# Kernel tuning notes

Hardware: AMD Instinct MI355X
Metric: run time of the kernel (lower is better)

## Reference

```python
import jax, jax.numpy as jnp
import numpy as np

B, N, D, H = 2, 256, 512, 8
DK = D // H


def _lin(x, w, b):
    # torch nn.Linear: y = x @ W.T + b, W is [out, in]
    return jnp.matmul(x, w.T) + b


def setup_inputs() -> dict:
    key = jax.random.key(0)
    ks = jax.random.split(key, 12)
    std = 0.02
    inp = {
        "x": jax.random.normal(ks[0], (B, N, D), jnp.float32),
        "batched_graphs": jax.random.normal(ks[1], (B, N, N, D), jnp.float32) * std,
        "mask": jnp.zeros((B, N, N), dtype=bool),
    }
    names = ["wq", "wk", "wv", "wo", "wl", "wr", "wrk", "wrv"]
    for i, n in enumerate(names):
        inp[n] = jax.random.normal(ks[2 + i], (D, D), jnp.float32) * std
        inp["b" + n[1:]] = jnp.zeros((D,), jnp.float32)
    return inp


def reference(x, batched_graphs, mask,
              wq, bq, wk, bk, wv, bv, wo, bo,
              wl, bl, wr, br, wrk, brk, wrv, brv):
    # update_relations: per-edge key/value maps
    graphs_k = _lin(batched_graphs, wrk, brk).reshape(B, N, N, H, DK)
    graphs_v = _lin(batched_graphs, wrv, brv).reshape(B, N, N, H, DK)

    query = _lin(x, wq, bq).reshape(B, N, H, DK)
    key_ = _lin(x, wk, bk).reshape(B, N, H, DK)
    value = _lin(x, wv, bv).reshape(B, N, H, DK)

    scores_k = jnp.einsum("bxhd,byhd->bxyh", query, key_)
    scores_g = jnp.einsum("bxhd,bxyhd->bxyh", query, graphs_k)
    scores = (scores_k + scores_g) / np.sqrt(DK).astype(np.float32)
    scores = jnp.where(mask[..., None], jnp.float32(-1e9), scores)
    p_attn = jax.nn.softmax(scores, axis=2)  # over key nodes y

    x_v = jnp.einsum("bxyh,byhd->bxhd", p_attn, value)
    x_g = jnp.einsum("bxyh,bxyhd->bxhd", p_attn, graphs_v)
    out = (x_v + x_g).reshape(B, N, D)

    # relation update: outer sum of left/right projections
    x_left = _lin(out, wl, bl)[:, :, None, :]   # [B,N,1,D]
    x_right = _lin(out, wr, br)[:, None, :, :]  # [B,1,N,D]
    new_graphs = x_left + x_right               # [B,N,N,D]

    return _lin(out, wo, bo), new_graphs
```

## Files before the change

### kernel.cpp

```cpp
#include <hip/hip_runtime.h>

#define BB 2
#define NN 256
#define DD 512
#define HH 8

__device__ __forceinline__ float dot4(float4 a, float4 b) {
    return a.x*b.x + a.y*b.y + a.z*b.z + a.w*b.w;
}

__device__ __forceinline__ void gload_lds16(const void* g, void* l) {
    __builtin_amdgcn_global_load_lds(
        (const __attribute__((address_space(1))) unsigned int*)g,
        (__attribute__((address_space(3))) unsigned int*)l, 16, 0, 0);
}

__device__ __forceinline__ void stage_swz(const char* rowbase, float4* dst, int w, int lane) {
    #pragma unroll
    for (int j = 0; j < 4; ++j) {
        const int f0 = w * 256 + j * 64;
        const int y = f0 >> 7;
        const int c = (f0 & 127) + lane;
        gload_lds16(rowbase + (size_t)y * 2048 + ((size_t)(c ^ y) << 4), &dst[f0]);
    }
}

__global__ __launch_bounds__(256) void kProj(
    const float* __restrict__ in_,
    const float* __restrict__ w0, const float* __restrict__ b0,
    const float* __restrict__ w1, const float* __restrict__ b1,
    const float* __restrict__ w2, const float* __restrict__ b2,
    float* __restrict__ o0, float* __restrict__ o1, float* __restrict__ o2)
{
    __shared__ float4 xs[2][32 * 17];
    __shared__ float4 ws[2][32 * 17];

    const int t = threadIdx.x;
    const int blk = blockIdx.x;
    const int proj = blk >> 8;
    const int rem = blk & 255;
    const int row0 = (rem >> 4) * 32;
    const int col0 = (rem & 15) * 32;

    const float* W; const float* Bp; float* O;
    if (proj == 0)      { W = w0; Bp = b0; O = o0; }
    else if (proj == 1) { W = w1; Bp = b1; O = o1; }
    else                { W = w2; Bp = b2; O = o2; }

    const int sr0 = t >> 4,          se0 = t & 15;
    const int sr1 = (t + 256) >> 4,  se1 = t & 15;
    const float4* X4 = (const float4*)in_;
    const float4* W4 = (const float4*)W;

    float4 rx0 = X4[(size_t)(row0 + sr0) * 128 + se0];
    float4 rx1 = X4[(size_t)(row0 + sr1) * 128 + se1];
    float4 rw0 = W4[(size_t)(col0 + sr0) * 128 + se0];
    float4 rw1 = W4[(size_t)(col0 + sr1) * 128 + se1];
    xs[0][sr0 * 17 + se0] = rx0;
    xs[0][sr1 * 17 + se1] = rx1;
    ws[0][sr0 * 17 + se0] = rw0;
    ws[0][sr1 * 17 + se1] = rw1;

    const int ty = t >> 4, tx = t & 15;
    const int ra = 2 * ty, ca = 2 * tx;
    float a00 = 0, a01 = 0, a10 = 0, a11 = 0;

    for (int q = 0; q < 8; ++q) {
        __syncthreads();
        const int cur = q & 1;
        if (q < 7) {
            const int koff = (q + 1) * 16;
            rx0 = X4[(size_t)(row0 + sr0) * 128 + koff + se0];
            rx1 = X4[(size_t)(row0 + sr1) * 128 + koff + se1];
            rw0 = W4[(size_t)(col0 + sr0) * 128 + koff + se0];
            rw1 = W4[(size_t)(col0 + sr1) * 128 + koff + se1];
        }
        const float4* xb = xs[cur];
        const float4* wb = ws[cur];
        #pragma unroll
        for (int e4 = 0; e4 < 16; ++e4) {
            const float4 x0 = xb[ra * 17 + e4];
            const float4 x1 = xb[(ra + 1) * 17 + e4];
            const float4 v0 = wb[ca * 17 + e4];
            const float4 v1 = wb[(ca + 1) * 17 + e4];
            a00 += dot4(x0, v0); a01 += dot4(x0, v1);
            a10 += dot4(x1, v0); a11 += dot4(x1, v1);
        }
        if (q < 7) {
            const int nxt = cur ^ 1;
            xs[nxt][sr0 * 17 + se0] = rx0;
            xs[nxt][sr1 * 17 + se1] = rx1;
            ws[nxt][sr0 * 17 + se0] = rw0;
            ws[nxt][sr1 * 17 + se1] = rw1;
        }
    }

    const int orow = row0 + ra, ocol = col0 + ca;
    const float bx = Bp[ocol], by = Bp[ocol + 1];
    float2 s0; s0.x = a00 + bx; s0.y = a01 + by;
    float2 s1; s1.x = a10 + bx; s1.y = a11 + by;
    *(float2*)(O + (size_t)orow * DD + ocol) = s0;
    *(float2*)(O + (size_t)(orow + 1) * DD + ocol) = s1;
}

__global__ __launch_bounds__(256) void kQkp(
    const float* __restrict__ q, const float* __restrict__ wrk,
    float* __restrict__ qkp)
{
    __shared__ float qs[8 * 64];
    const int t = threadIdx.x;
    const int blk = blockIdx.x;
    const int rowg = blk >> 5;
    const int h = (blk >> 2) & 7;
    const int eq = blk & 3;
    const int row0 = rowg * 8;
    {
        const int r = t >> 5, d2 = (t & 31) * 2;
        const float2 tmp = *(const float2*)(q + (size_t)(row0 + r) * DD + h * 64 + d2);
        qs[r * 64 + d2] = tmp.x; qs[r * 64 + d2 + 1] = tmp.y;
    }
    __syncthreads();
    const int e = eq * 128 + (t & 127);
    const int rp = (t >> 7) * 4;
    const float* wcol = wrk + (size_t)(h * 64) * DD + e;
    float a0 = 0, a1 = 0, a2 = 0, a3 = 0;
    #pragma unroll 8
    for (int d = 0; d < 64; ++d) {
        const float wv = wcol[(size_t)d * DD];
        a0 += qs[(rp + 0) * 64 + d] * wv;
        a1 += qs[(rp + 1) * 64 + d] * wv;
        a2 += qs[(rp + 2) * 64 + d] * wv;
        a3 += qs[(rp + 3) * 64 + d] * wv;
    }
    qkp[((size_t)(row0 + rp + 0) * HH + h) * DD + e] = a0;
    qkp[((size_t)(row0 + rp + 1) * HH + h) * DD + e] = a1;
    qkp[((size_t)(row0 + rp + 2) * HH + h) * DD + e] = a2;
    qkp[((size_t)(row0 + rp + 3) * HH + h) * DD + e] = a3;
}

__global__ __launch_bounds__(256) void kSk(
    const float* __restrict__ q, const float* __restrict__ k,
    const unsigned char* __restrict__ mask, float* __restrict__ sk)
{
    __shared__ float qs[8 * 65];
    __shared__ float ks[64 * 65];
    const int t = threadIdx.x;
    const int blk = blockIdx.x;
    const int b  = blk >> 10;
    const int h  = (blk >> 7) & 7;
    const int xt = (blk >> 2) & 31;
    const int yt = blk & 3;
    const int x0 = xt * 8, y0 = yt * 64;
    {
        const int r = t >> 5, d2 = (t & 31) * 2;
        const float2 tmp = *(const float2*)(q + (size_t)(b * NN + x0 + r) * DD + h * 64 + d2);
        qs[r * 65 + d2] = tmp.x; qs[r * 65 + d2 + 1] = tmp.y;
    }
    #pragma unroll
    for (int j = 0; j < 8; ++j) {
        const int f = t + 256 * j;
        const int r = f >> 5, d2 = (f & 31) * 2;
        const float2 tmp = *(const float2*)(k + (size_t)(b * NN + y0 + r) * DD + h * 64 + d2);
        ks[r * 65 + d2] = tmp.x; ks[r * 65 + d2 + 1] = tmp.y;
    }
    __syncthreads();
    const int xi = t >> 5, yg = t & 31;
    float a0 = 0, a1 = 0;
    #pragma unroll 8
    for (int d = 0; d < 64; ++d) {
        const float qv = qs[xi * 65 + d];
        a0 += qv * ks[(yg * 2 + 0) * 65 + d];
        a1 += qv * ks[(yg * 2 + 1) * 65 + d];
    }
    a0 *= 0.125f; a1 *= 0.125f;
    const unsigned char* mrow = mask + (size_t)(b * NN + x0 + xi) * NN;
    const int gy = y0 + yg * 2;
    if (mrow[gy + 0]) a0 = -1e9f;
    if (mrow[gy + 1]) a1 = -1e9f;
    float2 st; st.x = a0; st.y = a1;
    *(float2*)(sk + ((size_t)(b * NN + x0 + xi) * HH + h) * NN + gy) = st;
}

__global__ __launch_bounds__(256) void kC(
    const float* __restrict__ G, const float* __restrict__ sk,
    const float* __restrict__ qkp, const float* __restrict__ v,
    float* __restrict__ pg, float* __restrict__ pxv,
    float* __restrict__ pm, float* __restrict__ pl)
{
    __shared__ float4 gbuf[2][1024];
    __shared__ float4 qk4[1024];
    __shared__ float s_l[64];

    const int t = threadIdx.x;
    const int lane = t & 63;
    const int w = t >> 6;
    const int blk = blockIdx.x;
    const int part = blk & 3;
    const int bid = blk >> 2;
    const int b = bid >> 8;
    const int ybase = part * 64;

    const char* Grow = (const char*)(G + (size_t)bid * NN * DD);
    stage_swz((const char*)(qkp + (size_t)bid * HH * DD), qk4, w, lane);
    stage_swz(Grow + (size_t)ybase * 2048, &gbuf[0][0], w, lane);
    __syncthreads();

    const int s_  = t & 15;
    const int h0i = ((t >> 4) & 3) * 2;
    const int y0i = w * 2;
    const int ec4 = t & 127;
    const int hb  = (t >> 7) * 4;
    const int hv  = t >> 5;
    const int d2  = (t & 31) * 2;

    float4 gacc0 = {0,0,0,0}, gacc1 = {0,0,0,0}, gacc2 = {0,0,0,0}, gacc3 = {0,0,0,0};
    float m0 = -3e38f, m1 = -3e38f, m2 = -3e38f, m3 = -3e38f;
    float l0 = 0, l1 = 0, l2 = 0, l3 = 0;
    float vx = 0, vy = 0, mvold = -3e38f;

    const float* vrow = v + (size_t)(b * NN + ybase) * DD + hv * 64 + d2;
    const float* skrow = sk + (size_t)bid * HH * NN;

    int cb = 0;
    for (int tt = 0; tt < 8; ++tt) {
        if (tt < 7)
            stage_swz(Grow + (size_t)(ybase + (tt + 1) * 8) * 2048, &gbuf[cb ^ 1][0], w, lane);

        {
            float a00 = 0, a01 = 0, a10 = 0, a11 = 0;
            const float4* gb = &gbuf[cb][0];
            #pragma unroll
            for (int i = 0; i < 8; ++i) {
                const int e4 = i * 16 + s_;
                const float4 g0 = gb[y0i * 128 + (e4 ^ y0i)];
                const float4 g1 = gb[(y0i + 1) * 128 + (e4 ^ (y0i + 1))];
                const float4 p0 = qk4[h0i * 128 + (e4 ^ h0i)];
                const float4 p1 = qk4[(h0i + 1) * 128 + (e4 ^ (h0i + 1))];
                a00 += dot4(g0, p0); a01 += dot4(g0, p1);
                a10 += dot4(g1, p0); a11 += dot4(g1, p1);
            }
            #pragma unroll
            for (int mm = 1; mm < 16; mm <<= 1) {
                a00 += __shfl_xor(a00, mm); a01 += __shfl_xor(a01, mm);
                a10 += __shfl_xor(a10, mm); a11 += __shfl_xor(a11, mm);
            }
            if (s_ < 4) {
                const int yy = s_ & 1, hh = s_ >> 1;
                const float val = yy ? (hh ? a11 : a10) : (hh ? a01 : a00);
                const int gy = ybase + tt * 8 + y0i + yy;
                const int h = h0i + hh;
                s_l[(y0i + yy) * 8 + h] = val * 0.125f + skrow[(size_t)h * NN + gy];
            }
        }
        __syncthreads();

        {
            {   const float tmx0 = fmaxf(fmaxf(fmaxf(s_l[0*8+hb+0], s_l[1*8+hb+0]), fmaxf(s_l[2*8+hb+0], s_l[3*8+hb+0])),
                                         fmaxf(fmaxf(s_l[4*8+hb+0], s_l[5*8+hb+0]), fmaxf(s_l[6*8+hb+0], s_l[7*8+hb+0])));
                const float mn = fmaxf(m0, tmx0); const float rs = __expf(m0 - mn);
                m0 = mn; l0 *= rs; gacc0.x *= rs; gacc0.y *= rs; gacc0.z *= rs; gacc0.w *= rs; }
            {   const float tmx1 = fmaxf(fmaxf(fmaxf(s_l[0*8+hb+1], s_l[1*8+hb+1]), fmaxf(s_l[2*8+hb+1], s_l[3*8+hb+1])),
                                         fmaxf(fmaxf(s_l[4*8+hb+1], s_l[5*8+hb+1]), fmaxf(s_l[6*8+hb+1], s_l[7*8+hb+1])));
                const float mn = fmaxf(m1, tmx1); const float rs = __expf(m1 - mn);
                m1 = mn; l1 *= rs; gacc1.x *= rs; gacc1.y *= rs; gacc1.z *= rs; gacc1.w *= rs; }
            {   const float tmx2 = fmaxf(fmaxf(fmaxf(s_l[0*8+hb+2], s_l[1*8+hb+2]), fmaxf(s_l[2*8+hb+2], s_l[3*8+hb+2])),
                                         fmaxf(fmaxf(s_l[4*8+hb+2], s_l[5*8+hb+2]), fmaxf(s_l[6*8+hb+2], s_l[7*8+hb+2])));
                const float mn = fmaxf(m2, tmx2); const float rs = __expf(m2 - mn);
                m2 = mn; l2 *= rs; gacc2.x *= rs; gacc2.y *= rs; gacc2.z *= rs; gacc2.w *= rs; }
            {   const float tmx3 = fmaxf(fmaxf(fmaxf(s_l[0*8+hb+3], s_l[1*8+hb+3]), fmaxf(s_l[2*8+hb+3], s_l[3*8+hb+3])),
                                         fmaxf(fmaxf(s_l[4*8+hb+3], s_l[5*8+hb+3]), fmaxf(s_l[6*8+hb+3], s_l[7*8+hb+3])));
                const float mn = fmaxf(m3, tmx3); const float rs = __expf(m3 - mn);
                m3 = mn; l3 *= rs; gacc3.x *= rs; gacc3.y *= rs; gacc3.z *= rs; gacc3.w *= rs; }

            const int ri = hv & 3;
            const float mv = (ri & 2) ? ((ri & 1) ? m3 : m2) : ((ri & 1) ? m1 : m0);
            const float rv = __expf(mvold - mv);
            vx *= rv; vy *= rv; mvold = mv;

            const float4* gb = &gbuf[cb][0];
            const float* vt = vrow + (size_t)tt * 8 * DD;
            #pragma unroll
            for (int y = 0; y < 8; ++y) {
                const float4 gv = gb[y * 128 + (ec4 ^ y)];
                const float2 vv = *(const float2*)(vt + (size_t)y * DD);
                const float p0 = __expf(s_l[y*8 + hb + 0] - m0); l0 += p0;
                gacc0.x += p0*gv.x; gacc0.y += p0*gv.y; gacc0.z += p0*gv.z; gacc0.w += p0*gv.w;
                const float p1 = __expf(s_l[y*8 + hb + 1] - m1); l1 += p1;
                gacc1.x += p1*gv.x; gacc1.y += p1*gv.y; gacc1.z += p1*gv.z; gacc1.w += p1*gv.w;
                const float p2 = __expf(s_l[y*8 + hb + 2] - m2); l2 += p2;
                gacc2.x += p2*gv.x; gacc2.y += p2*gv.y; gacc2.z += p2*gv.z; gacc2.w += p2*gv.w;
                const float p3 = __expf(s_l[y*8 + hb + 3] - m3); l3 += p3;
                gacc3.x += p3*gv.x; gacc3.y += p3*gv.y; gacc3.z += p3*gv.z; gacc3.w += p3*gv.w;
                const float pv = __expf(s_l[y*8 + hv] - mv);
                vx += pv * vv.x; vy += pv * vv.y;
            }
        }
        __syncthreads();
        cb ^= 1;
    }

    float4* pgb = (float4*)pg + (size_t)blk * 1024;
    pgb[(hb + 0) * 128 + ec4] = gacc0;
    pgb[(hb + 1) * 128 + ec4] = gacc1;
    pgb[(hb + 2) * 128 + ec4] = gacc2;
    pgb[(hb + 3) * 128 + ec4] = gacc3;
    float2 xvst; xvst.x = vx; xvst.y = vy;
    *(float2*)(pxv + (size_t)blk * DD + hv * 64 + d2) = xvst;
    if ((t & 127) == 0) {
        const int base = blk * 8 + hb;
        pm[base + 0] = m0; pm[base + 1] = m1; pm[base + 2] = m2; pm[base + 3] = m3;
        pl[base + 0] = l0; pl[base + 1] = l1; pl[base + 2] = l2; pl[base + 3] = l3;
    }
}

__global__ __launch_bounds__(256) void kM(
    const float* __restrict__ pg, const float* __restrict__ pxv,
    const float* __restrict__ pm, const float* __restrict__ pl,
    const float* __restrict__ wrv, const float* __restrict__ brv,
    float* __restrict__ om)
{
    __shared__ float4 gc[512];
    __shared__ float xvs[256];
    __shared__ float wexp[16], Ls[4];
    const int t = threadIdx.x;
    const int blk = blockIdx.x;
    const int bid = blk >> 1;
    const int half = blk & 1;
    const int h0 = half * 4;
    __shared__ float mlds[16], llds[16];
    if (t < 16) {
        const int i = t >> 2, hh = t & 3;
        mlds[t] = pm[bid * 32 + i * 8 + h0 + hh];
        llds[t] = pl[bid * 32 + i * 8 + h0 + hh];
    }
    __syncthreads();
    if (t < 4) {
        float M = mlds[t];
        #pragma unroll
        for (int i = 1; i < 4; ++i) M = fmaxf(M, mlds[i * 4 + t]);
        float L = 0;
        #pragma unroll
        for (int i = 0; i < 4; ++i) {
            const float wv = __expf(mlds[i * 4 + t] - M);
            wexp[i * 4 + t] = wv;
            L += wv * llds[i * 4 + t];
        }
        Ls[t] = L;
    }
    __syncthreads();
    const int c4 = t & 127;
    #pragma unroll
    for (int r = 0; r < 2; ++r) {
        const int hh = (t >> 7) * 2 + r;
        float4 acc = {0, 0, 0, 0};
        #pragma unroll
        for (int i = 0; i < 4; ++i) {
            const float wv = wexp[i * 4 + hh];
            const float4 g = ((const float4*)pg)[((size_t)bid * 4 + i) * 1024 + (size_t)(h0 + hh) * 128 + c4];
            acc.x += wv * g.x; acc.y += wv * g.y; acc.z += wv * g.z; acc.w += wv * g.w;
        }
        gc[hh * 128 + c4] = acc;
    }
    {
        const int hh = t >> 6;
        float s = 0;
        #pragma unroll
        for (int i = 0; i < 4; ++i)
            s += wexp[i * 4 + hh] * pxv[((size_t)bid * 4 + i) * DD + half * 256 + t];
        xvs[t] = s;
    }
    __syncthreads();
    const int o = half * 256 + t;
    const int hl = t >> 6;
    const float4* wr4 = (const float4*)(wrv + (size_t)o * DD);
    float acc = 0;
    #pragma unroll 4
    for (int e4 = 0; e4 < 128; ++e4) acc += dot4(wr4[e4], gc[hl * 128 + e4]);
    om[(size_t)bid * DD + o] = (xvs[t] + acc) / Ls[hl] + brv[o];
}

__global__ __launch_bounds__(256) void kE(
    const float* __restrict__ xl, const float* __restrict__ xr,
    float* __restrict__ ng)
{
    const int t = threadIdx.x;
    const int blk = blockIdx.x;
    const int bid = blk >> 2;
    const int yc = blk & 3;
    const int b = bid >> 8;
    const int o4 = t & 127;
    const int yh = t >> 7;
    const float4 left = ((const float4*)xl)[(size_t)bid * 128 + o4];
    const float4* xr4 = (const float4*)xr + (size_t)b * NN * 128;
    float4* out4 = (float4*)ng + (size_t)bid * NN * 128;
    for (int y = yc * 64 + yh; y < yc * 64 + 64; y += 2) {
        const float4 rr = xr4[y * 128 + o4];
        float4 s;
        s.x = left.x + rr.x; s.y = left.y + rr.y;
        s.z = left.z + rr.z; s.w = left.w + rr.w;
        out4[y * 128 + o4] = s;
    }
}

extern "C" void kernel_launch(void* const* d_in, const int* in_sizes, int n_in,
                              void* d_out, int out_size, void* d_ws, size_t ws_size,
                              hipStream_t stream)
{
    (void)in_sizes; (void)n_in; (void)out_size; (void)ws_size;
    const float* x    = (const float*)d_in[0];
    const float* G    = (const float*)d_in[1];
    const unsigned char* mask = (const unsigned char*)d_in[2];
    const float* wq  = (const float*)d_in[3];  const float* bq  = (const float*)d_in[4];
    const float* wk  = (const float*)d_in[5];  const float* bk  = (const float*)d_in[6];
    const float* wv  = (const float*)d_in[7];  const float* bv  = (const float*)d_in[8];
    const float* wo  = (const float*)d_in[9];  const float* bo  = (const float*)d_in[10];
    const float* wl  = (const float*)d_in[11]; const float* bl  = (const float*)d_in[12];
    const float* wr  = (const float*)d_in[13]; const float* br  = (const float*)d_in[14];
    const float* wrk = (const float*)d_in[15];
    const float* wrv = (const float*)d_in[17]; const float* brv = (const float*)d_in[18];

    float* out  = (float*)d_out;
    float* fout = out;
    float* ng   = out + (size_t)BB * NN * DD;

    const size_t ng_f  = (size_t)BB * NN * NN * DD;
    const size_t row_f = (size_t)BB * NN * DD;
    const size_t total = row_f * 52 + 32768;
    float* base = ng + ng_f - total;
    float* q    = base;
    float* k    = q   + row_f;
    float* vv_  = k   + row_f;
    float* qkp  = vv_ + row_f;
    float* skp  = qkp + row_f * 8;
    float* pg   = skp + row_f * 4;
    float* pxv  = pg  + row_f * 32;
    float* pm   = pxv + row_f * 4;
    float* pl   = pm  + 16384;
    float* om   = pl  + 16384;
    float* xl = (float*)d_ws;
    float* xr = xl + row_f;

    kProj<<<768, 256, 0, stream>>>(x, wq, bq, wk, bk, wv, bv, q, k, vv_);
    kQkp <<<2048, 256, 0, stream>>>(q, wrk, qkp);
    kSk  <<<2048, 256, 0, stream>>>(q, k, mask, skp);
    kC   <<<2048, 256, 0, stream>>>(G, skp, qkp, vv_, pg, pxv, pm, pl);
    kM   <<<1024, 256, 0, stream>>>(pg, pxv, pm, pl, wrv, brv, om);
    kProj<<<768, 256, 0, stream>>>(om, wo, bo, wl, bl, wr, br, fout, xl, xr);
    kE   <<<2048, 256, 0, stream>>>(xl, xr, ng);
}
```

Before: 301.6 us.

## Keep query-graph vectors in registers, reuse softmax exps, nontemporal graph stores

In the attention kernel, each thread now loads its query/relation-key slices from global memory into registers, replacing the shared-memory staging buffer and its extra sync. The V rows for each tile are loaded into registers ahead of the score phase. The value-path probability reuses the exponent already computed for its head instead of a separate exp and rescale. Tile scores are read from LDS as float4. The outer-sum kernel writes new_graphs with nontemporal stores so the large output streams past the cache. The trade-off is higher register pressure, which could lower occupancy.

```diff
diff --git a/kernel.cpp b/kernel.cpp
--- a/kernel.cpp
+++ b/kernel.cpp
@@ -5,8 +5,15 @@
 #define DD 512
 #define HH 8
 
+typedef float f4raw __attribute__((ext_vector_type(4)));
+
 __device__ __forceinline__ float dot4(float4 a, float4 b) {
     return a.x*b.x + a.y*b.y + a.z*b.z + a.w*b.w;
+}
+
+__device__ __forceinline__ float4 f4fma(float s, float4 a, float4 acc) {
+    acc.x += s * a.x; acc.y += s * a.y; acc.z += s * a.z; acc.w += s * a.w;
+    return acc;
 }
 
 __device__ __forceinline__ void gload_lds16(const void* g, void* l) {
@@ -188,7 +195,6 @@
     float* __restrict__ pm, float* __restrict__ pl)
 {
     __shared__ float4 gbuf[2][1024];
-    __shared__ float4 qk4[1024];
     __shared__ float s_l[64];
 
     const int t = threadIdx.x;
@@ -201,9 +207,7 @@
     const int ybase = part * 64;
 
     const char* Grow = (const char*)(G + (size_t)bid * NN * DD);
-    stage_swz((const char*)(qkp + (size_t)bid * HH * DD), qk4, w, lane);
     stage_swz(Grow + (size_t)ybase * 2048, &gbuf[0][0], w, lane);
-    __syncthreads();
 
     const int s_  = t & 15;
     const int h0i = ((t >> 4) & 3) * 2;
@@ -212,19 +216,36 @@
     const int hb  = (t >> 7) * 4;
     const int hv  = t >> 5;
     const int d2  = (t & 31) * 2;
+    const int ri  = hv & 3;
+
+    const float* qkpb = qkp + (size_t)bid * HH * DD;
+    float4 qv0[8], qv1[8];
+    #pragma unroll
+    for (int i = 0; i < 8; ++i) {
+        const int e4 = i * 16 + s_;
+        qv0[i] = *(const float4*)(qkpb + (size_t)h0i * DD + e4 * 4);
+        qv1[i] = *(const float4*)(qkpb + (size_t)(h0i + 1) * DD + e4 * 4);
+    }
 
     float4 gacc0 = {0,0,0,0}, gacc1 = {0,0,0,0}, gacc2 = {0,0,0,0}, gacc3 = {0,0,0,0};
     float m0 = -3e38f, m1 = -3e38f, m2 = -3e38f, m3 = -3e38f;
     float l0 = 0, l1 = 0, l2 = 0, l3 = 0;
-    float vx = 0, vy = 0, mvold = -3e38f;
+    float vx = 0, vy = 0;
 
     const float* vrow = v + (size_t)(b * NN + ybase) * DD + hv * 64 + d2;
     const float* skrow = sk + (size_t)bid * HH * NN;
+
+    __syncthreads();
 
     int cb = 0;
     for (int tt = 0; tt < 8; ++tt) {
         if (tt < 7)
             stage_swz(Grow + (size_t)(ybase + (tt + 1) * 8) * 2048, &gbuf[cb ^ 1][0], w, lane);
+
+        float2 vvs[8];
+        #pragma unroll
+        for (int y = 0; y < 8; ++y)
+            vvs[y] = *(const float2*)(vrow + ((size_t)tt * 8 + y) * DD);
 
         {
             float a00 = 0, a01 = 0, a10 = 0, a11 = 0;
@@ -234,10 +255,8 @@
                 const int e4 = i * 16 + s_;
                 const float4 g0 = gb[y0i * 128 + (e4 ^ y0i)];
                 const float4 g1 = gb[(y0i + 1) * 128 + (e4 ^ (y0i + 1))];
-                const float4 p0 = qk4[h0i * 128 + (e4 ^ h0i)];
-                const float4 p1 = qk4[(h0i + 1) * 128 + (e4 ^ (h0i + 1))];
-                a00 += dot4(g0, p0); a01 += dot4(g0, p1);
-                a10 += dot4(g1, p0); a11 += dot4(g1, p1);
+                a00 += dot4(g0, qv0[i]); a01 += dot4(g0, qv1[i]);
+                a10 += dot4(g1, qv0[i]); a11 += dot4(g1, qv1[i]);
             }
             #pragma unroll
             for (int mm = 1; mm < 16; mm <<= 1) {
@@ -254,45 +273,41 @@
         }
         __syncthreads();
 
+        float4 sv[8];
+        #pragma unroll
+        for (int y = 0; y < 8; ++y) sv[y] = *(const float4*)&s_l[y * 8 + hb];
+
+        float4 mx = sv[0];
+        #pragma unroll
+        for (int y = 1; y < 8; ++y) {
+            mx.x = fmaxf(mx.x, sv[y].x); mx.y = fmaxf(mx.y, sv[y].y);
+            mx.z = fmaxf(mx.z, sv[y].z); mx.w = fmaxf(mx.w, sv[y].w);
+        }
+        const float n0 = fmaxf(m0, mx.x), rs0 = __expf(m0 - n0);
+        const float n1 = fmaxf(m1, mx.y), rs1 = __expf(m1 - n1);
+        const float n2 = fmaxf(m2, mx.z), rs2 = __expf(m2 - n2);
+        const float n3 = fmaxf(m3, mx.w), rs3 = __expf(m3 - n3);
+        m0 = n0; m1 = n1; m2 = n2; m3 = n3;
+        l0 *= rs0; l1 *= rs1; l2 *= rs2; l3 *= rs3;
+        gacc0.x *= rs0; gacc0.y *= rs0; gacc0.z *= rs0; gacc0.w *= rs0;
+        gacc1.x *= rs1; gacc1.y *= rs1; gacc1.z *= rs1; gacc1.w *= rs1;
+        gacc2.x *= rs2; gacc2.y *= rs2; gacc2.z *= rs2; gacc2.w *= rs2;
+        gacc3.x *= rs3; gacc3.y *= rs3; gacc3.z *= rs3; gacc3.w *= rs3;
+        const float rsv = (ri == 0) ? rs0 : (ri == 1) ? rs1 : (ri == 2) ? rs2 : rs3;
+        vx *= rsv; vy *= rsv;
+
         {
-            {   const float tmx0 = fmaxf(fmaxf(fmaxf(s_l[0*8+hb+0], s_l[1*8+hb+0]), fmaxf(s_l[2*8+hb+0], s_l[3*8+hb+0])),
-                                         fmaxf(fmaxf(s_l[4*8+hb+0], s_l[5*8+hb+0]), fmaxf(s_l[6*8+hb+0], s_l[7*8+hb+0])));
-                const float mn = fmaxf(m0, tmx0); const float rs = __expf(m0 - mn);
-                m0 = mn; l0 *= rs; gacc0.x *= rs; gacc0.y *= rs; gacc0.z *= rs; gacc0.w *= rs; }
-            {   const float tmx1 = fmaxf(fmaxf(fmaxf(s_l[0*8+hb+1], s_l[1*8+hb+1]), fmaxf(s_l[2*8+hb+1], s_l[3*8+hb+1])),
-                                         fmaxf(fmaxf(s_l[4*8+hb+1], s_l[5*8+hb+1]), fmaxf(s_l[6*8+hb+1], s_l[7*8+hb+1])));
-                const float mn = fmaxf(m1, tmx1); const float rs = __expf(m1 - mn);
-                m1 = mn; l1 *= rs; gacc1.x *= rs; gacc1.y *= rs; gacc1.z *= rs; gacc1.w *= rs; }
-            {   const float tmx2 = fmaxf(fmaxf(fmaxf(s_l[0*8+hb+2], s_l[1*8+hb+2]), fmaxf(s_l[2*8+hb+2], s_l[3*8+hb+2])),
-                                         fmaxf(fmaxf(s_l[4*8+hb+2], s_l[5*8+hb+2]), fmaxf(s_l[6*8+hb+2], s_l[7*8+hb+2])));
-                const float mn = fmaxf(m2, tmx2); const float rs = __expf(m2 - mn);
-                m2 = mn; l2 *= rs; gacc2.x *= rs; gacc2.y *= rs; gacc2.z *= rs; gacc2.w *= rs; }
-            {   const float tmx3 = fmaxf(fmaxf(fmaxf(s_l[0*8+hb+3], s_l[1*8+hb+3]), fmaxf(s_l[2*8+hb+3], s_l[3*8+hb+3])),
-                                         fmaxf(fmaxf(s_l[4*8+hb+3], s_l[5*8+hb+3]), fmaxf(s_l[6*8+hb+3], s_l[7*8+hb+3])));
-                const float mn = fmaxf(m3, tmx3); const float rs = __expf(m3 - mn);
-                m3 = mn; l3 *= rs; gacc3.x *= rs; gacc3.y *= rs; gacc3.z *= rs; gacc3.w *= rs; }
-
-            const int ri = hv & 3;
-            const float mv = (ri & 2) ? ((ri & 1) ? m3 : m2) : ((ri & 1) ? m1 : m0);
-            const float rv = __expf(mvold - mv);
-            vx *= rv; vy *= rv; mvold = mv;
-
             const float4* gb = &gbuf[cb][0];
-            const float* vt = vrow + (size_t)tt * 8 * DD;
             #pragma unroll
             for (int y = 0; y < 8; ++y) {
                 const float4 gv = gb[y * 128 + (ec4 ^ y)];
-                const float2 vv = *(const float2*)(vt + (size_t)y * DD);
-                const float p0 = __expf(s_l[y*8 + hb + 0] - m0); l0 += p0;
-                gacc0.x += p0*gv.x; gacc0.y += p0*gv.y; gacc0.z += p0*gv.z; gacc0.w += p0*gv.w;
-                const float p1 = __expf(s_l[y*8 + hb + 1] - m1); l1 += p1;
-                gacc1.x += p1*gv.x; gacc1.y += p1*gv.y; gacc1.z += p1*gv.z; gacc1.w += p1*gv.w;
-                const float p2 = __expf(s_l[y*8 + hb + 2] - m2); l2 += p2;
-                gacc2.x += p2*gv.x; gacc2.y += p2*gv.y; gacc2.z += p2*gv.z; gacc2.w += p2*gv.w;
-                const float p3 = __expf(s_l[y*8 + hb + 3] - m3); l3 += p3;
-                gacc3.x += p3*gv.x; gacc3.y += p3*gv.y; gacc3.z += p3*gv.z; gacc3.w += p3*gv.w;
-                const float pv = __expf(s_l[y*8 + hv] - mv);
-                vx += pv * vv.x; vy += pv * vv.y;
+                const float4 s = sv[y];
+                const float p0 = __expf(s.x - m0); l0 += p0; gacc0 = f4fma(p0, gv, gacc0);
+                const float p1 = __expf(s.y - m1); l1 += p1; gacc1 = f4fma(p1, gv, gacc1);
+                const float p2 = __expf(s.z - m2); l2 += p2; gacc2 = f4fma(p2, gv, gacc2);
+                const float p3 = __expf(s.w - m3); l3 += p3; gacc3 = f4fma(p3, gv, gacc3);
+                const float pv = (ri == 0) ? p0 : (ri == 1) ? p1 : (ri == 2) ? p2 : p3;
+                vx += pv * vvs[y].x; vy += pv * vvs[y].y;
             }
         }
         __syncthreads();
@@ -392,13 +407,13 @@
     const int yh = t >> 7;
     const float4 left = ((const float4*)xl)[(size_t)bid * 128 + o4];
     const float4* xr4 = (const float4*)xr + (size_t)b * NN * 128;
-    float4* out4 = (float4*)ng + (size_t)bid * NN * 128;
+    f4raw* out4 = (f4raw*)ng + (size_t)bid * NN * 128;
     for (int y = yc * 64 + yh; y < yc * 64 + 64; y += 2) {
         const float4 rr = xr4[y * 128 + o4];
-        float4 s;
+        f4raw s;
         s.x = left.x + rr.x; s.y = left.y + rr.y;
         s.z = left.z + rr.z; s.w = left.w + rr.w;
-        out4[y * 128 + o4] = s;
+        __builtin_nontemporal_store(s, &out4[y * 128 + o4]);
     }
 }
 
```

Measured after the change: 297.0 us. Within noise of the previous version (-1.5%).
